# Kernel tuning notes

Measured on AMD Instinct MI355X. Metric: run time of the kernel, lower is better.

## Reference

```python
import jax, jax.numpy as jnp
import numpy as np
import math

NUM_HEADS = 16
HIDDEN = 1024
HEAD = HIDDEN // NUM_HEADS


def setup_inputs() -> dict:
    key = jax.random.key(0)
    ks = jax.random.split(key, 11)
    B, S, H = 2, 2048, HIDDEN
    s = 1.0 / math.sqrt(H)
    return {
        "q": jax.random.normal(ks[0], (B, S, H), jnp.float32),
        "k": jax.random.normal(ks[1], (B, S, H), jnp.float32),
        "v": jax.random.normal(ks[2], (B, S, H), jnp.float32),
        "Wq": jax.random.normal(ks[3], (H, H), jnp.float32) * s,
        "bq": jnp.zeros((H,), jnp.float32),
        "Wk": jax.random.normal(ks[4], (H, H), jnp.float32) * s,
        "bk": jnp.zeros((H,), jnp.float32),
        "Wv": jax.random.normal(ks[5], (H, H), jnp.float32) * s,
        "bv": jnp.zeros((H,), jnp.float32),
        "Wo": jax.random.normal(ks[6], (H, H), jnp.float32) * s,
        "bo": jnp.zeros((H,), jnp.float32),
    }


def reference(q, k, v, Wq, bq, Wk, bk, Wv, bv, Wo, bo):
    B, S, H = q.shape
    nh, hd = NUM_HEADS, HEAD
    # projections (torch Linear: x @ W.T + b)
    qp = (q @ Wq.T + bq).reshape(B, S, nh, hd).transpose(0, 2, 1, 3)  # [B,nh,S,hd]
    kp = (k @ Wk.T + bk).reshape(B, S, nh, hd).transpose(0, 2, 1, 3)
    vp = (v @ Wv.T + bv).reshape(B, S, nh, hd).transpose(0, 2, 1, 3)
    scores = jnp.einsum('bhqd,bhkd->bhqk', qp, kp) / math.sqrt(hd)
    attn = jax.nn.softmax(scores, axis=-1)  # [B,nh,S,S]
    o = jnp.einsum('bhqk,bhkd->bhqd', attn, vp)
    o = o.transpose(0, 2, 1, 3).reshape(B, S, H)
    return o @ Wo.T + bo
```

## Files before the change

### kernel.cpp

```cpp
#include <hip/hip_runtime.h>
#include <cstdint>
#include <type_traits>
#include <utility>

typedef __attribute__((ext_vector_type(8))) short short8;
typedef __attribute__((ext_vector_type(8))) _Float16 f16x8_t;
typedef __attribute__((ext_vector_type(4))) float f32x4;

template <typename V, typename = void>
struct mfma_h_takes : std::false_type {};
template <typename V>
struct mfma_h_takes<V, std::void_t<decltype(__builtin_amdgcn_mfma_f32_16x16x32_f16(
    std::declval<V>(), std::declval<V>(), std::declval<f32x4>(), 0, 0, 0))>>
    : std::true_type {};

using hfrag_t = std::conditional_t<mfma_h_takes<f16x8_t>::value, f16x8_t, short8>;
static_assert(mfma_h_takes<f16x8_t>::value || mfma_h_takes<short8>::value,
              "no usable mfma_f32_16x16x32_f16 signature");

__device__ __forceinline__ f32x4 mfma16h(hfrag_t a, hfrag_t b, f32x4 c) {
  return __builtin_amdgcn_mfma_f32_16x16x32_f16(a, b, c, 0, 0, 0);
}

__device__ __forceinline__ void gld_lds16(const void* g, void* l) {
  __builtin_amdgcn_global_load_lds(
      (const __attribute__((address_space(1))) void*)(uintptr_t)g,
      (__attribute__((address_space(3))) void*)(uint32_t)(uintptr_t)l, 16, 0, 0);
}

__device__ __forceinline__ uint16_t f16_rne(float x) {
  return __builtin_bit_cast(uint16_t, (_Float16)x);
}
__device__ __forceinline__ float f16_up(uint16_t h) {
  return (float)__builtin_bit_cast(_Float16, h);
}

__device__ __forceinline__ float exp2_fast(float x) {
#if __has_builtin(__builtin_amdgcn_exp2f)
  return __builtin_amdgcn_exp2f(x);
#else
  return exp2f(x);
#endif
}
__device__ __forceinline__ uint32_t pk_f16(float a, float b) {
#if __has_builtin(__builtin_amdgcn_cvt_pkrtz)
  return __builtin_bit_cast(uint32_t, __builtin_amdgcn_cvt_pkrtz(a, b));
#else
  union { uint16_t u[2]; uint32_t w; } r;
  r.u[0] = f16_rne(a);
  r.u[1] = f16_rne(b);
  return r.w;
#endif
}

__device__ __forceinline__ int swz(int row, int col) {
  return row * 64 + ((((col >> 3) + row) & 7) << 3) + (col & 7);
}

struct SplitArgs {
  const float* src[4];
  uint16_t* hi[4];
  uint16_t* lo[4];
  int n4;
};
__global__ void split_multi(SplitArgs a) {
  const int z = blockIdx.y;
  int i = blockIdx.x * 256 + threadIdx.x;
  if (i >= a.n4) return;
  float4 x = ((const float4*)a.src[z])[i];
  ushort4 h;
  h.x = f16_rne(x.x);
  h.y = f16_rne(x.y);
  h.z = f16_rne(x.z);
  h.w = f16_rne(x.w);
  ((ushort4*)a.hi[z])[i] = h;
  if (a.lo[z]) {
    ushort4 l;
    l.x = f16_rne(x.x - f16_up(h.x));
    l.y = f16_rne(x.y - f16_up(h.y));
    l.z = f16_rne(x.z - f16_up(h.z));
    l.w = f16_rne(x.w - f16_up(h.w));
    ((ushort4*)a.lo[z])[i] = l;
  }
}

struct QKVArgs {
  const uint16_t* Ah[3];
  const uint16_t* Bh[3];
  const float* bias[3];
  uint16_t* oH[3];
  uint16_t* oL[3];
};

__global__ __launch_bounds__(256, 2) void gemm_qkv(QKVArgs args) {
  __shared__ uint16_t lds[2][2][128][64];
  const int K = 1024;
  const int tid = threadIdx.x;
  const int wv = tid >> 6, lane = tid & 63;
  const int lm = lane & 15, g = lane >> 4;
  const int wm = (wv & 1) * 64, wn = (wv >> 1) * 64;
  const int z = blockIdx.z;
  const bool isT = (z == 2);
  const int t = blockIdx.x + 8 * blockIdx.y;
  const int kx = t & 7, j = t >> 3;
  const int sx = (j & 3) | ((kx & 1) << 2);
  const int sy = (j >> 2) | ((kx >> 1) << 3);
  const int gm0 = (isT ? sx : sy) * 128;
  const int gn0 = (isT ? sy : sx) * 128;

  const uint16_t* base[2] = {args.Ah[z] + (size_t)gm0 * K,
                             args.Bh[z] + (size_t)gn0 * K};
  const int rl8 = lane >> 3;
  const int scl = (((lane & 7) - rl8) & 7) * 8;

  f32x4 acc[4][4];
#pragma unroll
  for (int a = 0; a < 4; ++a)
#pragma unroll
    for (int b = 0; b < 4; ++b) acc[a][b] = (f32x4)0.0f;

#pragma unroll
  for (int jj = 0; jj < 8; ++jj) {
    const int c = wv + 4 * jj;
    const int p = c >> 4, r8 = (c & 15) * 8;
    gld_lds16(base[p] + (size_t)(r8 + rl8) * K + 0 + scl, &lds[0][p][r8][0]);
  }

#pragma unroll 1
  for (int ti = 0; ti < 16; ++ti) {
    const int cur = ti & 1;
    if (ti + 1 < 16) {
      const int kt = (ti + 1) * 64;
#pragma unroll
      for (int jj = 0; jj < 8; ++jj) {
        const int c = wv + 4 * jj;
        const int p = c >> 4, r8 = (c & 15) * 8;
        gld_lds16(base[p] + (size_t)(r8 + rl8) * K + kt + scl,
                  &lds[cur ^ 1][p][r8][0]);
      }
      asm volatile("s_waitcnt vmcnt(8)" ::: "memory");
    } else {
      asm volatile("s_waitcnt vmcnt(0)" ::: "memory");
    }
    __builtin_amdgcn_sched_barrier(0);
    __builtin_amdgcn_s_barrier();
    __builtin_amdgcn_sched_barrier(0);
#pragma unroll
    for (int ks = 0; ks < 2; ++ks) {
      const int uc = ((ks * 4 + g + lm) & 7) * 8;
      hfrag_t af[4];
#pragma unroll
      for (int mf = 0; mf < 4; ++mf) {
        af[mf] = *(const hfrag_t*)&lds[cur][0][wm + mf * 16 + lm][uc];
      }
#pragma unroll
      for (int nf = 0; nf < 4; ++nf) {
        hfrag_t bhf = *(const hfrag_t*)&lds[cur][1][wn + nf * 16 + lm][uc];
#pragma unroll
        for (int mf = 0; mf < 4; ++mf) {
          acc[mf][nf] = mfma16h(af[mf], bhf, acc[mf][nf]);
        }
      }
    }
    __builtin_amdgcn_sched_barrier(0);
    __builtin_amdgcn_s_barrier();
    __builtin_amdgcn_sched_barrier(0);
  }
  const float* bias = args.bias[z];
  uint16_t* oH = args.oH[z];
  uint16_t* oL = args.oL[z];
  const float kQScale = 0.18033688f;
#pragma unroll
  for (int mf = 0; mf < 4; ++mf) {
#pragma unroll
    for (int nf = 0; nf < 4; ++nf) {
      const int col = gn0 + wn + nf * 16 + lm;
#pragma unroll
      for (int i = 0; i < 4; ++i) {
        const int row = gm0 + wm + mf * 16 + g * 4 + i;
        float v = acc[mf][nf][i] + (isT ? bias[row] : bias[col]);
        if (z == 0) v *= kQScale;
        uint16_t h = f16_rne(v);
        size_t addr;
        if (!isT) {
          addr = ((size_t)((row >> 11) * 16 + (col >> 6)) * 2048 + (row & 2047)) * 64 +
                 (col & 63);
        } else {
          addr = ((size_t)((col >> 11) * 1024 + row)) * 2048 + (col & 2047);
        }
        oH[addr] = h;
        if (oL) oL[addr] = f16_rne(v - f16_up(h));
      }
    }
  }
}

__global__ __launch_bounds__(256, 2) void gemm_o(
    const uint16_t* __restrict__ Ah, const uint16_t* __restrict__ Bh,
    const float* __restrict__ bias, float* __restrict__ out) {
  const int K = 1024, N = 1024;
  __shared__ uint16_t ldsA[2][64][64];
  __shared__ uint16_t ldsB[2][128][64];
  const int tid = threadIdx.x;
  const int wv = tid >> 6, lane = tid & 63;
  const int lm = lane & 15, g = lane >> 4;
  const int wm = (wv & 1) * 32, wn = (wv >> 1) * 64;
  const int t = blockIdx.x + 8 * blockIdx.y;
  const int kx = t & 7, j = t >> 3;
  const int sx = (j & 3) | ((kx & 1) << 2);
  const int sy = (j >> 2) | ((kx >> 1) << 4);
  const int gm0 = sy * 64, gn0 = sx * 128;
  const uint16_t* baseA = Ah + (size_t)gm0 * K;
  const uint16_t* baseB = Bh + (size_t)gn0 * K;
  const int rl8 = lane >> 3;
  const int scl = (((lane & 7) - rl8) & 7) * 8;

  f32x4 acc[2][4];
#pragma unroll
  for (int a = 0; a < 2; ++a)
#pragma unroll
    for (int b = 0; b < 4; ++b) acc[a][b] = (f32x4)0.0f;

#pragma unroll
  for (int jj = 0; jj < 6; ++jj) {
    const int c = wv + 4 * jj;
    if (c < 8) {
      gld_lds16(baseA + (size_t)(c * 8 + rl8) * K + 0 + scl, &ldsA[0][c * 8][0]);
    } else {
      const int b = c - 8;
      gld_lds16(baseB + (size_t)(b * 8 + rl8) * K + 0 + scl, &ldsB[0][b * 8][0]);
    }
  }

#pragma unroll 1
  for (int ti = 0; ti < 16; ++ti) {
    const int cur = ti & 1;
    if (ti + 1 < 16) {
      const int kt = (ti + 1) * 64;
#pragma unroll
      for (int jj = 0; jj < 6; ++jj) {
        const int c = wv + 4 * jj;
        if (c < 8) {
          gld_lds16(baseA + (size_t)(c * 8 + rl8) * K + kt + scl,
                    &ldsA[cur ^ 1][c * 8][0]);
        } else {
          const int b = c - 8;
          gld_lds16(baseB + (size_t)(b * 8 + rl8) * K + kt + scl,
                    &ldsB[cur ^ 1][b * 8][0]);
        }
      }
      asm volatile("s_waitcnt vmcnt(6)" ::: "memory");
    } else {
      asm volatile("s_waitcnt vmcnt(0)" ::: "memory");
    }
    __builtin_amdgcn_sched_barrier(0);
    __builtin_amdgcn_s_barrier();
    __builtin_amdgcn_sched_barrier(0);
#pragma unroll
    for (int ks = 0; ks < 2; ++ks) {
      const int uc = ((ks * 4 + g + lm) & 7) * 8;
      hfrag_t af[2];
#pragma unroll
      for (int mf = 0; mf < 2; ++mf) {
        af[mf] = *(const hfrag_t*)&ldsA[cur][wm + mf * 16 + lm][uc];
      }
#pragma unroll
      for (int nf = 0; nf < 4; ++nf) {
        hfrag_t bhf = *(const hfrag_t*)&ldsB[cur][wn + nf * 16 + lm][uc];
#pragma unroll
        for (int mf = 0; mf < 2; ++mf) {
          acc[mf][nf] = mfma16h(af[mf], bhf, acc[mf][nf]);
        }
      }
    }
    __builtin_amdgcn_sched_barrier(0);
    __builtin_amdgcn_s_barrier();
    __builtin_amdgcn_sched_barrier(0);
  }
#pragma unroll
  for (int mf = 0; mf < 2; ++mf)
#pragma unroll
    for (int nf = 0; nf < 4; ++nf) {
      const int col = gn0 + wn + nf * 16 + lm;
#pragma unroll
      for (int i = 0; i < 4; ++i) {
        const int row = gm0 + wm + mf * 16 + g * 4 + i;
        out[(size_t)row * N + col] = acc[mf][nf][i] + bias[col];
      }
    }
}

__global__ __launch_bounds__(256, 2) void attn_kernel(
    const uint16_t* __restrict__ Qh,
    const uint16_t* __restrict__ Kh,
    const uint16_t* __restrict__ Vh,
    float* __restrict__ opart, float* __restrict__ lpart) {
  __shared__ uint16_t kt[4096];
  __shared__ uint16_t vt[4096];
  __shared__ uint16_t pp[8192];
  const int tid = threadIdx.x;
  const int wave = tid >> 6, lane = tid & 63;
  const int lm = lane & 15, g = lane >> 4;
  const int linear = blockIdx.x + 32 * blockIdx.y;
  const int bh = (linear & 7) + 8 * (linear >> 8);
  const int qt = (linear >> 3) & 15;
  const int half = (linear >> 7) & 1;
  const int kvh = half * 1024;
  const size_t base = (size_t)bh * 131072;
  const int q0 = qt * 128 + wave * 32;

  hfrag_t qf[2][2];
#pragma unroll
  for (int b = 0; b < 2; ++b) {
    const size_t rb = base + (size_t)(q0 + b * 16 + lm) * 64 + g * 8;
    qf[b][0] = *(const hfrag_t*)(Qh + rb);
    qf[b][1] = *(const hfrag_t*)(Qh + rb + 32);
  }
  f32x4 oacc[2][4];
  f32x4 lacc[2];
#pragma unroll
  for (int mf = 0; mf < 2; ++mf) {
    lacc[mf] = (f32x4)0.0f;
#pragma unroll
    for (int nf = 0; nf < 4; ++nf) oacc[mf][nf] = (f32x4)0.0f;
  }
  short8 ones_s = (short8)(short)0x3C00;
  hfrag_t ones = __builtin_bit_cast(hfrag_t, ones_s);

  const int sr = tid >> 3;
  const int sc = (tid & 7) * 8;

  uint4 kr0, kr1, vr0, vr1;
  {
    const size_t ka = base + (size_t)(kvh + sr) * 64 + sc;
    kr0 = *(const uint4*)(Kh + ka);
    kr1 = *(const uint4*)(Kh + ka + 2048);
  }

#pragma unroll 1
  for (int it = 0; it < 16; ++it) {
    const int kv0 = kvh + it * 64;
    *(uint4*)&kt[swz(sr, sc)] = kr0;
    *(uint4*)&kt[swz(sr + 32, sc)] = kr1;
    __syncthreads();
    {
      const size_t va = base + (size_t)sr * 2048 + kv0 + sc;
      vr0 = *(const uint4*)(Vh + va);
      vr1 = *(const uint4*)(Vh + va + 65536);
    }
    if (it + 1 < 16) {
      const size_t ka = base + (size_t)(kv0 + 64 + sr) * 64 + sc;
      kr0 = *(const uint4*)(Kh + ka);
      kr1 = *(const uint4*)(Kh + ka + 2048);
    }
    f32x4 sct[4][2];
#pragma unroll
    for (int a = 0; a < 4; ++a)
#pragma unroll
      for (int b = 0; b < 2; ++b) sct[a][b] = (f32x4)0.0f;
    __builtin_amdgcn_s_setprio(1);
#pragma unroll
    for (int ks = 0; ks < 2; ++ks) {
#pragma unroll
      for (int a = 0; a < 4; ++a) {
        hfrag_t kfh = *(const hfrag_t*)&kt[swz(a * 16 + lm, ks * 32 + g * 8)];
#pragma unroll
        for (int b = 0; b < 2; ++b) {
          sct[a][b] = mfma16h(kfh, qf[b][ks], sct[a][b]);
        }
      }
    }
    __builtin_amdgcn_s_setprio(0);
#pragma unroll
    for (int a = 0; a < 4; ++a) {
#pragma unroll
      for (int b = 0; b < 2; ++b) {
        float e0 = exp2_fast(fminf(sct[a][b][0], 15.0f));
        float e1 = exp2_fast(fminf(sct[a][b][1], 15.0f));
        float e2 = exp2_fast(fminf(sct[a][b][2], 15.0f));
        float e3 = exp2_fast(fminf(sct[a][b][3], 15.0f));
        uint2 pk;
        pk.x = pk_f16(e0, e1);
        pk.y = pk_f16(e2, e3);
        *(uint2*)&pp[swz(wave * 32 + b * 16 + lm, a * 16 + g * 4)] = pk;
      }
    }
    *(uint4*)&vt[swz(sr, sc)] = vr0;
    *(uint4*)&vt[swz(sr + 32, sc)] = vr1;
    __syncthreads();
    __builtin_amdgcn_s_setprio(1);
#pragma unroll
    for (int ks = 0; ks < 2; ++ks) {
      hfrag_t pa[2];
#pragma unroll
      for (int mf = 0; mf < 2; ++mf) {
        pa[mf] = *(const hfrag_t*)&pp[swz(wave * 32 + mf * 16 + lm, ks * 32 + g * 8)];
        lacc[mf] = mfma16h(pa[mf], ones, lacc[mf]);
      }
#pragma unroll
      for (int nf = 0; nf < 4; ++nf) {
        hfrag_t vbh = *(const hfrag_t*)&vt[swz(nf * 16 + lm, ks * 32 + g * 8)];
#pragma unroll
        for (int mf = 0; mf < 2; ++mf) {
          oacc[mf][nf] = mfma16h(pa[mf], vbh, oacc[mf][nf]);
        }
      }
    }
    __builtin_amdgcn_s_setprio(0);
  }
  const int obase = (half * 32 + bh) * 2048;
#pragma unroll
  for (int mf = 0; mf < 2; ++mf) {
#pragma unroll
    for (int i = 0; i < 4; ++i) {
      const int qrow = qt * 128 + wave * 32 + mf * 16 + g * 4 + i;
      float* orow = opart + ((size_t)obase + qrow) * 64;
#pragma unroll
      for (int nf = 0; nf < 4; ++nf) orow[nf * 16 + lm] = oacc[mf][nf][i];
      if (lm == 0) lpart[obase + qrow] = lacc[mf][i];
    }
  }
}

__global__ void combine_kernel(const float* __restrict__ opart,
                               const float* __restrict__ lpart,
                               uint16_t* __restrict__ oh) {
  const int idx = blockIdx.x * 256 + threadIdx.x;
  const float4 a = ((const float4*)opart)[idx];
  const float4 b = ((const float4*)(opart + 4194304))[idx];
  const int row = idx >> 4;
  const float linv = 1.0f / (lpart[row] + lpart[65536 + row]);
  const int bh = row >> 11, qq = row & 2047;
  const int bb = bh >> 4, hh = bh & 15;
  const size_t o = ((size_t)(bb * 2048 + qq)) * 1024 + hh * 64 + (idx & 15) * 4;
  ushort4 H;
  H.x = f16_rne((a.x + b.x) * linv);
  H.y = f16_rne((a.y + b.y) * linv);
  H.z = f16_rne((a.z + b.z) * linv);
  H.w = f16_rne((a.w + b.w) * linv);
  *(ushort4*)(oh + o) = H;
}

extern "C" void kernel_launch(void* const* d_in, const int* in_sizes, int n_in,
                              void* d_out, int out_size, void* d_ws, size_t ws_size,
                              hipStream_t stream) {
  const float* q = (const float*)d_in[0];
  const float* k = (const float*)d_in[1];
  const float* v = (const float*)d_in[2];
  const float* Wq = (const float*)d_in[3];
  const float* bq = (const float*)d_in[4];
  const float* Wk = (const float*)d_in[5];
  const float* bk = (const float*)d_in[6];
  const float* Wv = (const float*)d_in[7];
  const float* bv = (const float*)d_in[8];
  const float* Wo = (const float*)d_in[9];
  const float* bo = (const float*)d_in[10];

  const size_t NX = 4194304;
  const size_t NW = 1048576;
  uint16_t* p = (uint16_t*)d_ws;
  uint16_t* xqh = p; p += NX; uint16_t* xql = p; p += NX;
  uint16_t* xkh = p; p += NX; uint16_t* xkl = p; p += NX;
  uint16_t* xvh = p; p += NX; uint16_t* xvl = p; p += NX;
  uint16_t* wqh = p; p += NW; uint16_t* wql = p; p += NW;
  uint16_t* wkh = p; p += NW; uint16_t* wkl = p; p += NW;
  uint16_t* wvh = p; p += NW; uint16_t* wvl = p; p += NW;
  uint16_t* woh = p; p += NW; uint16_t* wol = p; p += NW;
  uint16_t* qph = p; p += NX; uint16_t* qpl = p; p += NX;
  uint16_t* kph = p; p += NX; uint16_t* kpl = p; p += NX;
  uint16_t* vth = p; p += NX; uint16_t* vtl = p; p += NX;
  uint16_t* oh = xqh;
  float* opart = (float*)xkh;
  float* lpart = opart + 2 * 4194304;

  SplitArgs sx;
  sx.src[0] = q;  sx.hi[0] = xqh; sx.lo[0] = nullptr;
  sx.src[1] = k;  sx.hi[1] = xkh; sx.lo[1] = nullptr;
  sx.src[2] = v;  sx.hi[2] = xvh; sx.lo[2] = nullptr;
  sx.src[3] = nullptr; sx.hi[3] = nullptr; sx.lo[3] = nullptr;
  sx.n4 = (int)(NX / 4);
  split_multi<<<dim3((unsigned)(NX / 4 / 256), 3), 256, 0, stream>>>(sx);

  SplitArgs sw;
  sw.src[0] = Wq; sw.hi[0] = wqh; sw.lo[0] = nullptr;
  sw.src[1] = Wk; sw.hi[1] = wkh; sw.lo[1] = nullptr;
  sw.src[2] = Wv; sw.hi[2] = wvh; sw.lo[2] = nullptr;
  sw.src[3] = Wo; sw.hi[3] = woh; sw.lo[3] = nullptr;
  sw.n4 = (int)(NW / 4);
  split_multi<<<dim3((unsigned)(NW / 4 / 256), 4), 256, 0, stream>>>(sw);

  QKVArgs qa;
  qa.Ah[0] = xqh; qa.Bh[0] = wqh; qa.bias[0] = bq; qa.oH[0] = qph; qa.oL[0] = nullptr;
  qa.Ah[1] = xkh; qa.Bh[1] = wkh; qa.bias[1] = bk; qa.oH[1] = kph; qa.oL[1] = nullptr;
  qa.Ah[2] = wvh; qa.Bh[2] = xvh; qa.bias[2] = bv; qa.oH[2] = vth; qa.oL[2] = nullptr;
  gemm_qkv<<<dim3(8, 32, 3), 256, 0, stream>>>(qa);

  attn_kernel<<<dim3(32, 32), 256, 0, stream>>>(qph, kph, vth, opart, lpart);
  combine_kernel<<<4096, 256, 0, stream>>>(opart, lpart, oh);

  gemm_o<<<dim3(8, 64), 256, 0, stream>>>(oh, woh, bo, (float*)d_out);
}
```

Measured before the change: 237.6 us.

## Drop double-buffered LDS pipeline in QKV GEMM for single buffer and higher occupancy

Removes the double-buffered LDS prefetch in the QKV projection GEMM, switching to a single 32KB buffer with load-then-sync-compute-sync per K tile. The launch bounds go from 2 to 3 blocks per CU. The aim is to hide memory latency through more resident blocks rather than software prefetch. The risk is that global loads are no longer overlapped with MFMA work inside a block, and the tighter register budget could cause spills.

```diff
diff --git a/kernel.cpp b/kernel.cpp
--- a/kernel.cpp
+++ b/kernel.cpp
@@ -92,8 +92,8 @@
   uint16_t* oL[3];
 };
 
-__global__ __launch_bounds__(256, 2) void gemm_qkv(QKVArgs args) {
-  __shared__ uint16_t lds[2][2][128][64];
+__global__ __launch_bounds__(256, 3) void gemm_qkv(QKVArgs args) {
+  __shared__ uint16_t lds[2][128][64];
   const int K = 1024;
   const int tid = threadIdx.x;
   const int wv = tid >> 6, lane = tid & 63;
@@ -119,52 +119,33 @@
 #pragma unroll
     for (int b = 0; b < 4; ++b) acc[a][b] = (f32x4)0.0f;
 
-#pragma unroll
-  for (int jj = 0; jj < 8; ++jj) {
-    const int c = wv + 4 * jj;
-    const int p = c >> 4, r8 = (c & 15) * 8;
-    gld_lds16(base[p] + (size_t)(r8 + rl8) * K + 0 + scl, &lds[0][p][r8][0]);
-  }
-
 #pragma unroll 1
-  for (int ti = 0; ti < 16; ++ti) {
-    const int cur = ti & 1;
-    if (ti + 1 < 16) {
-      const int kt = (ti + 1) * 64;
-#pragma unroll
-      for (int jj = 0; jj < 8; ++jj) {
-        const int c = wv + 4 * jj;
-        const int p = c >> 4, r8 = (c & 15) * 8;
-        gld_lds16(base[p] + (size_t)(r8 + rl8) * K + kt + scl,
-                  &lds[cur ^ 1][p][r8][0]);
-      }
-      asm volatile("s_waitcnt vmcnt(8)" ::: "memory");
-    } else {
-      asm volatile("s_waitcnt vmcnt(0)" ::: "memory");
-    }
-    __builtin_amdgcn_sched_barrier(0);
-    __builtin_amdgcn_s_barrier();
-    __builtin_amdgcn_sched_barrier(0);
+  for (int kt = 0; kt < K; kt += 64) {
+#pragma unroll
+    for (int jj = 0; jj < 8; ++jj) {
+      const int c = wv + 4 * jj;
+      const int p = c >> 4, r8 = (c & 15) * 8;
+      gld_lds16(base[p] + (size_t)(r8 + rl8) * K + kt + scl, &lds[p][r8][0]);
+    }
+    __syncthreads();
 #pragma unroll
     for (int ks = 0; ks < 2; ++ks) {
       const int uc = ((ks * 4 + g + lm) & 7) * 8;
       hfrag_t af[4];
 #pragma unroll
       for (int mf = 0; mf < 4; ++mf) {
-        af[mf] = *(const hfrag_t*)&lds[cur][0][wm + mf * 16 + lm][uc];
+        af[mf] = *(const hfrag_t*)&lds[0][wm + mf * 16 + lm][uc];
       }
 #pragma unroll
       for (int nf = 0; nf < 4; ++nf) {
-        hfrag_t bhf = *(const hfrag_t*)&lds[cur][1][wn + nf * 16 + lm][uc];
+        hfrag_t bhf = *(const hfrag_t*)&lds[1][wn + nf * 16 + lm][uc];
 #pragma unroll
         for (int mf = 0; mf < 4; ++mf) {
           acc[mf][nf] = mfma16h(af[mf], bhf, acc[mf][nf]);
         }
       }
     }
-    __builtin_amdgcn_sched_barrier(0);
-    __builtin_amdgcn_s_barrier();
-    __builtin_amdgcn_sched_barrier(0);
+    __syncthreads();
   }
   const float* bias = args.bias[z];
   uint16_t* oH = args.oH[z];
```

New measurement: 239.4 us. No clear change (+0.8%).
